# Kernel tuning notes

Hardware: AMD Instinct MI355X
Metric: run time of the kernel (lower is better)

The kernel has to match this reference:

```python
import jax, jax.numpy as jnp
import numpy as np

DIM = 1024

def setup_inputs() -> dict:
    key = jax.random.key(0)
    k1, k2 = jax.random.split(key)
    X = jax.random.normal(k1, (4, 4096, DIM), dtype=jnp.float32)
    # nn.Linear(dim, 3*dim): weight [3*dim, dim], bias [3*dim]
    W = jax.random.normal(k2, (3 * DIM, DIM), dtype=jnp.float32) * (1.0 / np.sqrt(DIM))
    b = jnp.zeros((3 * DIM,), dtype=jnp.float32)
    return {"X": X, "W": W, "b": b}

def reference(X, W, b):
    dim = X.shape[-1]
    # fused QKV projection: [B,S,3D]
    QKV = jnp.einsum('bsd,ed->bse', X, W) + b
    Q, K, V = jnp.split(QKV, 3, axis=-1)
    scale = 1.0 / jnp.sqrt(jnp.asarray(dim, X.dtype))
    scores = jnp.einsum('bqd,bkd->bqk', Q, K) * scale  # [B,S,S]
    attn = jax.nn.softmax(scores, axis=-1)
    return jnp.einsum('bqk,bkd->bqd', attn, V)
```

## Files before the change

### kernel.cpp

```cpp
#include <hip/hip_runtime.h>
#include <cstdint>

typedef unsigned short u16;
typedef __attribute__((ext_vector_type(8))) short bf16x8;
typedef __attribute__((ext_vector_type(4))) float f32x4;

#define DIM   1024
#define BATCH 4
#define SEQ   4096
#define E3    3072
#define MTOT  (BATCH*SEQ)

__device__ __forceinline__ u16 f2bf(float x) {
    union { float f; unsigned u; } v; v.f = x;
    unsigned r = v.u + 0x7FFFu + ((v.u >> 16) & 1u);
    return (u16)(r >> 16);
}

__device__ __forceinline__ void gl16(const void* g, void* l) {
    __builtin_amdgcn_global_load_lds(
        (const __attribute__((address_space(1))) void*)g,
        (__attribute__((address_space(3))) void*)l, 16, 0, 0);
}

__device__ __forceinline__ void gemm256(
    const u16* __restrict__ A, int sA,
    const u16* __restrict__ B, int sB,
    int K, int m0, int n0,
    u16* lds, f32x4 acc[8][4])
{
    const int t   = threadIdx.x;
    const int w   = t >> 6, L = t & 63;
    const int rL  = L & 15, kq = L >> 4;
    const int qa  = 2*w;
    const int ia0 = 8*(w>>2);
    const int jb0 = 4*(w&3);

    const size_t ga0 = (size_t)(m0 + qa*16 + rL)*sA + kq*8;
    const size_t ga1 = ga0 + (size_t)16*sA;
    const size_t gb0 = (size_t)(n0 + qa*16 + rL)*sB + kq*8;
    const size_t gb1 = gb0 + (size_t)16*sB;

#define RING_STAGE(tile) { \
    const size_t k0 = (size_t)(tile)*32; \
    u16* sb = lds + ((tile)&3)*16384; \
    gl16(A + ga0 + k0, sb + qa*512); \
    gl16(A + ga1 + k0, sb + qa*512 + 512); \
    gl16(B + gb0 + k0, sb + 8192 + qa*512); \
    gl16(B + gb1 + k0, sb + 8192 + qa*512 + 512); }

#define RING_SYNC(N) \
    asm volatile("s_waitcnt vmcnt(" #N ")" ::: "memory"); \
    __builtin_amdgcn_s_barrier(); \
    asm volatile("" ::: "memory");

#define RING_COMPUTE(tile) { \
    const u16* sb = lds + ((tile)&3)*16384; \
    bf16x8 av[8], bv[4]; \
    _Pragma("unroll") \
    for (int i = 0; i < 8; ++i) av[i] = *(const bf16x8*)&sb[(ia0+i)*512 + L*8]; \
    _Pragma("unroll") \
    for (int j = 0; j < 4; ++j) bv[j] = *(const bf16x8*)&sb[8192 + (jb0+j)*512 + L*8]; \
    _Pragma("unroll") \
    for (int i = 0; i < 8; ++i) \
        _Pragma("unroll") \
        for (int j = 0; j < 4; ++j) \
            acc[i][j] = __builtin_amdgcn_mfma_f32_16x16x32_bf16(av[i], bv[j], acc[i][j], 0,0,0); }

    RING_STAGE(0); RING_STAGE(1); RING_STAGE(2);
    const int NT = K >> 5;
    for (int tt = 0; tt < NT-3; ++tt) {
        RING_SYNC(8);
        RING_STAGE(tt+3);
        RING_COMPUTE(tt);
    }
    RING_SYNC(8); RING_COMPUTE(NT-3);
    RING_SYNC(4); RING_COMPUTE(NT-2);
    RING_SYNC(0); RING_COMPUTE(NT-1);

#undef RING_STAGE
#undef RING_SYNC
#undef RING_COMPUTE
}

__global__ __launch_bounds__(256)
void cvt_bf16(const float* __restrict__ x, u16* __restrict__ y) {
    size_t i = ((size_t)blockIdx.x*256 + threadIdx.x)*4;
    float4 v = *(const float4*)&x[i];
    ushort4 h;
    h.x = f2bf(v.x); h.y = f2bf(v.y); h.z = f2bf(v.z); h.w = f2bf(v.w);
    *(ushort4*)&y[i] = h;
}

__global__ __launch_bounds__(512,2)
void gemm_qkv(const u16* __restrict__ Xbf, const u16* __restrict__ Wbf,
              const float* __restrict__ bias,
              u16* __restrict__ Qh, u16* __restrict__ Kh,
              u16* __restrict__ Vth)
{
    __shared__ __align__(16) u16 lds[65536];
    f32x4 acc[8][4];
    #pragma unroll
    for (int i=0;i<8;++i)
        #pragma unroll
        for (int j=0;j<4;++j) acc[i][j] = (f32x4){0.f,0.f,0.f,0.f};

    const int m0 = blockIdx.y*256, n0 = blockIdx.x*256;
    gemm256(Xbf, DIM, Wbf, DIM, DIM, m0, n0, lds, acc);

    const int t = threadIdx.x, w = t>>6, L = t&63;
    const int wm = 128*(w>>2), wn = 64*(w&3);
    const int cl = L&15, rq = (L>>4)*4;
    const int region = n0 >> 10;
    const float qscale = 0.03125f;

    if (region < 2) {
        u16* Dst = region ? Kh : Qh;
        const float fs = region ? 1.0f : qscale;
        #pragma unroll
        for (int j = 0; j < 4; ++j) {
            float bc = bias[n0 + wn + j*16 + cl];
            #pragma unroll
            for (int i = 0; i < 8; ++i)
                #pragma unroll
                for (int r = 0; r < 4; ++r)
                    acc[i][j][r] = (acc[i][j][r] + bc)*fs;
        }
        const int d0 = (n0 & 1023) + wn;
        #pragma unroll
        for (int p = 0; p < 2; ++p) {
            const int nt0 = 2*p, nt1 = 2*p+1;
            #pragma unroll
            for (int i = 0; i < 8; ++i) {
                int row0 = m0 + wm + i*16 + rq;
                int bi = row0 >> 12, s0 = row0 & (SEQ-1);
                #pragma unroll
                for (int r = 0; r < 4; ++r) {
                    float v0 = acc[i][nt0][r], v1 = acc[i][nt1][r];
                    float x0 = __shfl_xor(v0, 1, 64);
                    float x1 = __shfl_xor(v1, 1, 64);
                    unsigned wv; int colb;
                    if ((cl & 1) == 0) {
                        wv   = (unsigned)f2bf(v0) | ((unsigned)f2bf(x0) << 16);
                        colb = nt0*16 + cl;
                    } else {
                        wv   = (unsigned)f2bf(x1) | ((unsigned)f2bf(v1) << 16);
                        colb = nt1*16 + (cl-1);
                    }
                    size_t idx = ((size_t)bi*SEQ + s0 + r)*DIM + d0 + colb;
                    *(unsigned*)&Dst[idx] = wv;
                }
            }
        }
    } else {
        #pragma unroll
        for (int j = 0; j < 4; ++j) {
            int col = n0 + wn + j*16 + cl;
            float bc = bias[col];
            int d = col & (DIM-1);
            #pragma unroll
            for (int i = 0; i < 8; ++i) {
                int row0 = m0 + wm + i*16 + rq;
                int bi = row0 >> 12, s0 = row0 & (SEQ-1);
                ushort4 hv;
                hv.x = f2bf(acc[i][j][0] + bc);
                hv.y = f2bf(acc[i][j][1] + bc);
                hv.z = f2bf(acc[i][j][2] + bc);
                hv.w = f2bf(acc[i][j][3] + bc);
                size_t base = ((size_t)bi*DIM + d)*SEQ + s0;
                *(ushort4*)&Vth[base] = hv;
            }
        }
    }
}

__global__ __launch_bounds__(512,2)
void gemm_scores(const u16* __restrict__ Qh, const u16* __restrict__ Kh,
                 u16* __restrict__ S0, u16* __restrict__ S1,
                 u16* __restrict__ S2, u16* __restrict__ S3)
{
    __shared__ __align__(16) u16 lds[65536];
    f32x4 acc[8][4];
    #pragma unroll
    for (int i=0;i<8;++i)
        #pragma unroll
        for (int j=0;j<4;++j) acc[i][j] = (f32x4){0.f,0.f,0.f,0.f};

    const int bz = blockIdx.z;
    const size_t qo = (size_t)bz*SEQ*DIM;
    const int m0 = blockIdx.y*256, n0 = blockIdx.x*256;
    gemm256(Qh + qo, DIM, Kh + qo, DIM, DIM, m0, n0, lds, acc);

    u16* Sb = (bz == 0) ? S0 : (bz == 1) ? S1 : (bz == 2) ? S2 : S3;
    const int t = threadIdx.x, w = t>>6, L = t&63;
    const int wm = 128*(w>>2), wn = 64*(w&3);
    const int cl = L&15, rq = (L>>4)*4;
    #pragma unroll
    for (int p = 0; p < 2; ++p) {
        const int nt0 = 2*p, nt1 = 2*p+1;
        #pragma unroll
        for (int i = 0; i < 8; ++i) {
            int row0 = m0 + wm + i*16 + rq;
            #pragma unroll
            for (int r = 0; r < 4; ++r) {
                float v0 = acc[i][nt0][r], v1 = acc[i][nt1][r];
                float x0 = __shfl_xor(v0, 1, 64);
                float x1 = __shfl_xor(v1, 1, 64);
                unsigned wv; int colb;
                if ((cl & 1) == 0) {
                    wv   = (unsigned)f2bf(v0) | ((unsigned)f2bf(x0) << 16);
                    colb = nt0*16 + cl;
                } else {
                    wv   = (unsigned)f2bf(x1) | ((unsigned)f2bf(v1) << 16);
                    colb = nt1*16 + (cl-1);
                }
                *(unsigned*)&Sb[(size_t)(row0 + r)*SEQ + n0 + wn + colb] = wv;
            }
        }
    }
}

__global__ __launch_bounds__(256)
void softmax_pack(u16* __restrict__ S0, u16* __restrict__ S1,
                  u16* __restrict__ S2, u16* __restrict__ S3)
{
    __shared__ float red[4];
    const int t = threadIdx.x, L = t & 63, w = t >> 6;
    const int gr = blockIdx.x, bz = gr >> 12, rr = gr & (SEQ-1);
    u16* Sb = (bz == 0) ? S0 : (bz == 1) ? S1 : (bz == 2) ? S2 : S3;
    u16* row = Sb + (size_t)rr*SEQ;

    float v[16];
    float m = -1e30f;
    #pragma unroll
    for (int j = 0; j < 2; ++j) {
        ushort4 x0 = *(const ushort4*)&row[t*8 + j*2048];
        ushort4 x1 = *(const ushort4*)&row[t*8 + j*2048 + 4];
        union { unsigned u; float f; } c;
        c.u = (unsigned)x0.x << 16; v[8*j+0] = c.f;
        c.u = (unsigned)x0.y << 16; v[8*j+1] = c.f;
        c.u = (unsigned)x0.z << 16; v[8*j+2] = c.f;
        c.u = (unsigned)x0.w << 16; v[8*j+3] = c.f;
        c.u = (unsigned)x1.x << 16; v[8*j+4] = c.f;
        c.u = (unsigned)x1.y << 16; v[8*j+5] = c.f;
        c.u = (unsigned)x1.z << 16; v[8*j+6] = c.f;
        c.u = (unsigned)x1.w << 16; v[8*j+7] = c.f;
    }
    #pragma unroll
    for (int i = 0; i < 16; ++i) m = fmaxf(m, v[i]);
    #pragma unroll
    for (int off = 32; off; off >>= 1) m = fmaxf(m, __shfl_xor(m, off, 64));
    if (L == 0) red[w] = m;
    __syncthreads();
    m = fmaxf(fmaxf(red[0],red[1]), fmaxf(red[2],red[3]));

    float s = 0.f;
    #pragma unroll
    for (int i = 0; i < 16; ++i) { v[i] = __expf(v[i] - m); s += v[i]; }
    #pragma unroll
    for (int off = 32; off; off >>= 1) s += __shfl_xor(s, off, 64);
    __syncthreads();
    if (L == 0) red[w] = s;
    __syncthreads();
    s = red[0]+red[1]+red[2]+red[3];
    const float inv = 1.0f / s;

    #pragma unroll
    for (int j = 0; j < 2; ++j) {
        ushort4 h0, h1;
        h0.x = f2bf(v[8*j+0]*inv); h0.y = f2bf(v[8*j+1]*inv);
        h0.z = f2bf(v[8*j+2]*inv); h0.w = f2bf(v[8*j+3]*inv);
        h1.x = f2bf(v[8*j+4]*inv); h1.y = f2bf(v[8*j+5]*inv);
        h1.z = f2bf(v[8*j+6]*inv); h1.w = f2bf(v[8*j+7]*inv);
        *(ushort4*)&row[t*8 + j*2048]     = h0;
        *(ushort4*)&row[t*8 + j*2048 + 4] = h1;
    }
}

__global__ __launch_bounds__(512,2)
void gemm_pv(const u16* __restrict__ P0, const u16* __restrict__ P1,
             const u16* __restrict__ P2, const u16* __restrict__ P3,
             const u16* __restrict__ Vth,
             float* __restrict__ O0, float* __restrict__ O1,
             float* __restrict__ O2, float* __restrict__ O3)
{
    __shared__ __align__(16) u16 lds[65536];
    f32x4 acc[8][4];
    #pragma unroll
    for (int i=0;i<8;++i)
        #pragma unroll
        for (int j=0;j<4;++j) acc[i][j] = (f32x4){0.f,0.f,0.f,0.f};

    const int bz = blockIdx.z;
    const u16* Pb = (bz == 0) ? P0 : (bz == 1) ? P1 : (bz == 2) ? P2 : P3;
    float*     Ob = (bz == 0) ? O0 : (bz == 1) ? O1 : (bz == 2) ? O2 : O3;
    const int m0 = blockIdx.y*256, n0 = blockIdx.x*256;
    gemm256(Pb, SEQ, Vth + (size_t)bz*DIM*SEQ, SEQ, SEQ, m0, n0, lds, acc);

    const int t = threadIdx.x, w = t>>6, L = t&63;
    const int wm = 128*(w>>2), wn = 64*(w&3);
    const int cl = L&15, rq = (L>>4)*4;
    #pragma unroll
    for (int j = 0; j < 4; ++j) {
        int col = n0 + wn + j*16 + cl;
        #pragma unroll
        for (int i = 0; i < 8; ++i) {
            int row0 = m0 + wm + i*16 + rq;
            #pragma unroll
            for (int r = 0; r < 4; ++r)
                Ob[(size_t)(row0 + r)*DIM + col] = acc[i][j][r];
        }
    }
}

__global__ __launch_bounds__(256)
void copy_out(const float* __restrict__ src, float* __restrict__ dst)
{
    size_t i = ((size_t)blockIdx.x*256 + threadIdx.x)*4;
    *(float4*)&dst[i] = *(const float4*)&src[i];
}

extern "C" void kernel_launch(void* const* d_in, const int* in_sizes, int n_in,
                              void* d_out, int out_size, void* d_ws, size_t ws_size,
                              hipStream_t stream) {
    const float* X    = (const float*)d_in[0];
    const float* W    = (const float*)d_in[1];
    const float* bias = (const float*)d_in[2];
    float* out = (float*)d_out;

    const size_t MB = (size_t)1 << 20;
    if (ws_size < 192*MB) return;
    char* ws = (char*)d_ws;
    char* wo = (char*)d_out;
    u16* Qh  = (u16*)ws;
    u16* Kh  = (u16*)(ws + 32*MB);
    u16* Vth = (u16*)(ws + 64*MB);
    u16* S0  = (u16*)(ws + 96*MB);
    u16* S1  = (u16*)(ws + 128*MB);
    u16* S2  = (u16*)(ws + 160*MB);
    u16* Xbf = (u16*)wo;
    u16* Wbf = (u16*)(wo + 32*MB);
    u16* S3  = (u16*)(wo + 32*MB);
    float* O0 = (float*)wo;
    float* O1 = (float*)(wo + 16*MB);
    float* O2 = (float*)ws;
    float* O3 = (float*)(ws + 16*MB);

    cvt_bf16<<<MTOT*DIM/1024, 256, 0, stream>>>(X, Xbf);
    cvt_bf16<<<E3*DIM/1024,   256, 0, stream>>>(W, Wbf);

    gemm_qkv<<<dim3(E3/256, MTOT/256), 512, 0, stream>>>(
        Xbf, Wbf, bias, Qh, Kh, Vth);

    gemm_scores<<<dim3(SEQ/256, SEQ/256, BATCH), 512, 0, stream>>>(
        Qh, Kh, S0, S1, S2, S3);

    softmax_pack<<<MTOT, 256, 0, stream>>>(S0, S1, S2, S3);

    gemm_pv<<<dim3(DIM/256, SEQ/256, BATCH), 512, 0, stream>>>(
        S0, S1, S2, S3, Vth, O0, O1, O2, O3);

    copy_out<<<(32*MB/sizeof(float))/1024, 256, 0, stream>>>(
        (const float*)ws, out + 8*MB);
}
```

Baseline: 604.9 us.

## Split GEMM k-tile into two barriered phases with setprio around MFMA bursts

Restructures the gemm256 main loop so each k-tile is processed in two half-phases. Each phase loads half of the A fragments from LDS, issues half of the next tile's global-to-LDS loads, then runs a 4x4 MFMA burst at raised wave priority (s_setprio). Barriers between phases keep waves in lockstep so LDS reads, global loads and MFMA work from different waves interleave. The cost is twice as many barriers per tile and a tighter synchronisation schedule.

```diff
diff --git a/kernel.cpp b/kernel.cpp
--- a/kernel.cpp
+++ b/kernel.cpp
@@ -41,46 +41,76 @@
     const size_t gb0 = (size_t)(n0 + qa*16 + rL)*sB + kq*8;
     const size_t gb1 = gb0 + (size_t)16*sB;
 
-#define RING_STAGE(tile) { \
-    const size_t k0 = (size_t)(tile)*32; \
+    const int NT = K >> 5;
+    bf16x8 av[8], bv[4];
+
+#define STAGE_A(tile) { const size_t k0=(size_t)(tile)*32; \
     u16* sb = lds + ((tile)&3)*16384; \
     gl16(A + ga0 + k0, sb + qa*512); \
-    gl16(A + ga1 + k0, sb + qa*512 + 512); \
+    gl16(A + ga1 + k0, sb + qa*512 + 512); }
+#define STAGE_B(tile) { const size_t k0=(size_t)(tile)*32; \
+    u16* sb = lds + ((tile)&3)*16384; \
     gl16(B + gb0 + k0, sb + 8192 + qa*512); \
     gl16(B + gb1 + k0, sb + 8192 + qa*512 + 512); }
 
-#define RING_SYNC(N) \
-    asm volatile("s_waitcnt vmcnt(" #N ")" ::: "memory"); \
-    __builtin_amdgcn_s_barrier(); \
-    asm volatile("" ::: "memory");
-
-#define RING_COMPUTE(tile) { \
+#define MEMB  asm volatile("" ::: "memory")
+#define BAR   __builtin_amdgcn_s_barrier()
+#define LGKM0 asm volatile("s_waitcnt lgkmcnt(0)" ::: "memory")
+#define VM(n) asm volatile("s_waitcnt vmcnt(" #n ")" ::: "memory")
+
+#define PH0(tile, DOSTAGE) { \
     const u16* sb = lds + ((tile)&3)*16384; \
-    bf16x8 av[8], bv[4]; \
-    _Pragma("unroll") \
-    for (int i = 0; i < 8; ++i) av[i] = *(const bf16x8*)&sb[(ia0+i)*512 + L*8]; \
+    _Pragma("unroll") \
+    for (int i = 0; i < 4; ++i) av[i] = *(const bf16x8*)&sb[(ia0+i)*512 + L*8]; \
     _Pragma("unroll") \
     for (int j = 0; j < 4; ++j) bv[j] = *(const bf16x8*)&sb[8192 + (jb0+j)*512 + L*8]; \
-    _Pragma("unroll") \
-    for (int i = 0; i < 8; ++i) \
+    if (DOSTAGE) STAGE_A((tile)+3); \
+    MEMB; BAR; LGKM0; \
+    __builtin_amdgcn_s_setprio(1); \
+    _Pragma("unroll") \
+    for (int i = 0; i < 4; ++i) \
         _Pragma("unroll") \
         for (int j = 0; j < 4; ++j) \
-            acc[i][j] = __builtin_amdgcn_mfma_f32_16x16x32_bf16(av[i], bv[j], acc[i][j], 0,0,0); }
-
-    RING_STAGE(0); RING_STAGE(1); RING_STAGE(2);
-    const int NT = K >> 5;
+            acc[i][j] = __builtin_amdgcn_mfma_f32_16x16x32_bf16(av[i], bv[j], acc[i][j], 0,0,0); \
+    __builtin_amdgcn_s_setprio(0); \
+    MEMB; BAR; }
+
+#define PH1(tile, DOSTAGE, WAIT) { \
+    const u16* sb = lds + ((tile)&3)*16384; \
+    _Pragma("unroll") \
+    for (int i = 0; i < 4; ++i) av[4+i] = *(const bf16x8*)&sb[(ia0+4+i)*512 + L*8]; \
+    if (DOSTAGE) STAGE_B((tile)+3); \
+    MEMB; BAR; LGKM0; \
+    __builtin_amdgcn_s_setprio(1); \
+    _Pragma("unroll") \
+    for (int i = 0; i < 4; ++i) \
+        _Pragma("unroll") \
+        for (int j = 0; j < 4; ++j) \
+            acc[4+i][j] = __builtin_amdgcn_mfma_f32_16x16x32_bf16(av[4+i], bv[j], acc[4+i][j], 0,0,0); \
+    __builtin_amdgcn_s_setprio(0); \
+    WAIT; MEMB; BAR; }
+
+    STAGE_A(0); STAGE_B(0);
+    STAGE_A(1); STAGE_B(1);
+    STAGE_A(2); STAGE_B(2);
+    VM(8); BAR;
+
     for (int tt = 0; tt < NT-3; ++tt) {
-        RING_SYNC(8);
-        RING_STAGE(tt+3);
-        RING_COMPUTE(tt);
-    }
-    RING_SYNC(8); RING_COMPUTE(NT-3);
-    RING_SYNC(4); RING_COMPUTE(NT-2);
-    RING_SYNC(0); RING_COMPUTE(NT-1);
-
-#undef RING_STAGE
-#undef RING_SYNC
-#undef RING_COMPUTE
+        PH0(tt, 1);
+        PH1(tt, 1, VM(8));
+    }
+    PH0(NT-3, 0); PH1(NT-3, 0, VM(4));
+    PH0(NT-2, 0); PH1(NT-2, 0, VM(0));
+    PH0(NT-1, 0); PH1(NT-1, 0, (void)0);
+
+#undef STAGE_A
+#undef STAGE_B
+#undef PH0
+#undef PH1
+#undef MEMB
+#undef BAR
+#undef LGKM0
+#undef VM
 }
 
 __global__ __launch_bounds__(256)
```

New measurement: 615.4 us. Within noise of the previous version (+1.7%).
